# Kernel optimization log

Hardware: AMD Instinct MI355X
Metric: run time of the kernel (lower is better)

Reference implementation:

```python
import jax, jax.numpy as jnp
import numpy as np

B, S, D = 2, 1024, 4096          # batch, prefill seqlen, model dim
H, KVH, HD = 32, 8, 128          # q heads, kv heads, head dim
MAX = 2048                       # kv-cache capacity
THETA = 1000000.0
REP = H // KVH


def _rope_tables(pos):
    # pos: [S] int -> cos/sin [S, HD]
    inv_freq = 1.0 / (THETA ** (jnp.arange(0, HD, 2, dtype=jnp.float32) / HD))
    freqs = pos[:, None].astype(jnp.float32) * inv_freq[None, :]
    emb = jnp.concatenate([freqs, freqs], axis=-1)
    return jnp.cos(emb), jnp.sin(emb)


def _rotate_half(t):
    t1, t2 = jnp.split(t, 2, axis=-1)
    return jnp.concatenate([-t2, t1], axis=-1)


def setup_inputs() -> dict:
    key = jax.random.key(0)
    k = jax.random.split(key, 8)
    sc = 1.0 / np.sqrt(D)
    x = jax.random.normal(k[0], (B, S, D), jnp.float32)
    storage_idx = jnp.arange(S, dtype=jnp.int32)
    cache = jnp.zeros((2, 1, B, KVH, MAX, HD), jnp.float32)
    causal = jnp.tril(jnp.ones((MAX, MAX), bool))
    mask = jnp.where(causal, 0.0, -1e9).astype(jnp.float32)
    Wq = jax.random.normal(k[1], (D, H * HD), jnp.float32) * sc
    bq = jax.random.normal(k[2], (H * HD,), jnp.float32) * 0.01
    Wk = jax.random.normal(k[3], (D, KVH * HD), jnp.float32) * sc
    bk = jax.random.normal(k[4], (KVH * HD,), jnp.float32) * 0.01
    Wv = jax.random.normal(k[5], (D, KVH * HD), jnp.float32) * sc
    bv = jax.random.normal(k[6], (KVH * HD,), jnp.float32) * 0.01
    Wo = jax.random.normal(k[7], (H * HD, D), jnp.float32) * sc
    return {"x": x, "storage_idx": storage_idx, "cache": cache, "mask": mask,
            "Wq": Wq, "bq": bq, "Wk": Wk, "bk": bk, "Wv": Wv, "bv": bv, "Wo": Wo}


def reference(x, storage_idx, cache, mask, Wq, bq, Wk, bk, Wv, bv, Wo):
    bsz, seqlen, _ = x.shape
    # QKV projections -> [b, heads, s, hd]
    xq = (x @ Wq + bq).reshape(bsz, seqlen, H, HD).transpose(0, 2, 1, 3)
    xk = (x @ Wk + bk).reshape(bsz, seqlen, KVH, HD).transpose(0, 2, 1, 3)
    xv = (x @ Wv + bv).reshape(bsz, seqlen, KVH, HD).transpose(0, 2, 1, 3)
    # inline RoPE at positions storage_idx
    cos, sin = _rope_tables(storage_idx)       # [s, hd]
    cos = cos[None, None]                      # [1,1,s,hd]
    sin = sin[None, None]
    xq = xq * cos + _rotate_half(xq) * sin
    xk = xk * cos + _rotate_half(xk) * sin
    # KV-cache scatter (index_copy_ on dim -2 at storage_idx)
    keys = cache[0, 0].at[:, :, storage_idx, :].set(xk)    # [b, kvh, MAX, hd]
    values = cache[1, 0].at[:, :, storage_idx, :].set(xv)
    # GQA: repeat kv heads
    keys = jnp.repeat(keys, REP, axis=1)       # [b, H, MAX, hd]
    values = jnp.repeat(values, REP, axis=1)
    # attention with additive mask rows gathered at storage_idx
    scores = jnp.einsum('bhqd,bhkd->bhqk', xq, keys) / np.sqrt(HD)
    scores = scores + mask[storage_idx][None, None]        # [b, H, s, MAX]
    attn = jax.nn.softmax(scores, axis=-1)
    out = jnp.einsum('bhqk,bhkd->bhqd', attn, values)
    out = out.transpose(0, 2, 1, 3).reshape(bsz, seqlen, H * HD)
    return out @ Wo
```

## Files before the change

kernel.cpp:

```cpp
#include <hip/hip_runtime.h>
#include <hip/hip_bf16.h>

typedef unsigned short u16;
typedef unsigned int   u32;
using bf16x8 = __attribute__((ext_vector_type(8))) short;
using f32x4  = __attribute__((ext_vector_type(4))) float;
using f32x16 = __attribute__((ext_vector_type(16))) float;

#define AS1 __attribute__((address_space(1)))
#define AS3 __attribute__((address_space(3)))

static constexpr int S_   = 1024;
static constexpr int D_   = 4096;
static constexpr int H_   = 32;
static constexpr int KVH_ = 8;
static constexpr int HD_  = 128;
static constexpr int NQKV = H_*HD_ + 2*KVH_*HD_;

__device__ __forceinline__ u16 f2bf(float f) {
  union { float f; u32 u; } v; v.f = f;
  u32 r = v.u + 0x7FFFu + ((v.u >> 16) & 1u);
  return (u16)(r >> 16);
}

__global__ void k_convert(const float* __restrict__ src, u16* __restrict__ dst, int n4) {
  int i = blockIdx.x * blockDim.x + threadIdx.x;
  if (i >= n4) return;
  float4 v = ((const float4*)src)[i];
  ushort4 o;
  o.x = f2bf(v.x); o.y = f2bf(v.y); o.z = f2bf(v.z); o.w = f2bf(v.w);
  ((ushort4*)dst)[i] = o;
}

__global__ __launch_bounds__(256) void k_transpose_all(
    const float* __restrict__ Wq, const float* __restrict__ Wk,
    const float* __restrict__ Wv, const float* __restrict__ Wo,
    u16* __restrict__ WB, u16* __restrict__ WoT) {
  constexpr int K = 4096;
  __shared__ float t[64][65];
  int id = blockIdx.x;
  const float* src; u16* dst; int N, tx, ty, perm;
  if (id < 4096)      { src = Wq; dst = WB;                        N = 4096; tx = id & 63; ty = id >> 6; perm = 1; }
  else if (id < 5120) { id -= 4096; src = Wk; dst = WB + (size_t)4096*K; N = 1024; tx = id & 15; ty = id >> 4; perm = 1; }
  else if (id < 6144) { id -= 5120; src = Wv; dst = WB + (size_t)5120*K; N = 1024; tx = id & 15; ty = id >> 4; perm = 0; }
  else                { id -= 6144; src = Wo; dst = WoT;           N = 4096; tx = id & 63; ty = id >> 6; perm = 0; }
  int k0 = ty * 64, n0 = tx * 64;
  int tid = threadIdx.x;
  int srcb[4];
#pragma unroll
  for (int g = 0; g < 4; ++g) {
    int np = n0 + g*16;
    if (perm) {
      int f = (np >> 4) & 7, m = f >> 1;
      srcb[g] = (np & ~127) + ((f & 1) ? 64 + m*16 : m*16);
    } else srcb[g] = np;
  }
  int lr = tid >> 4;
  int lc = (tid & 15) * 4;
  int scol = srcb[lc >> 4] + (lc & 15);
#pragma unroll
  for (int i = 0; i < 4; ++i) {
    float4 v = *(const float4*)&src[(size_t)(k0 + lr + i*16) * N + scol];
    t[lc+0][lr + i*16] = v.x;
    t[lc+1][lr + i*16] = v.y;
    t[lc+2][lr + i*16] = v.z;
    t[lc+3][lr + i*16] = v.w;
  }
  __syncthreads();
  int wn = tid >> 3;
  int wk = (tid & 7) * 8;
#pragma unroll
  for (int i = 0; i < 2; ++i) {
    const float* row = &t[wn + i*32][wk];
    ushort4 a, b;
    a.x = f2bf(row[0]); a.y = f2bf(row[1]); a.z = f2bf(row[2]); a.w = f2bf(row[3]);
    b.x = f2bf(row[4]); b.y = f2bf(row[5]); b.z = f2bf(row[6]); b.w = f2bf(row[7]);
    u16* o = &dst[(size_t)(n0 + wn + i*32) * K + k0 + wk];
    *(ushort4*)o = a;
    *(ushort4*)(o + 4) = b;
  }
}

__global__ void k_transpose_v(const u16* __restrict__ src, u16* __restrict__ dst) {
  __shared__ u16 t[32][33];
  int bg = blockIdx.z;
  int s0 = blockIdx.x * 32, h0 = blockIdx.y * 32;
  src += (size_t)bg * S_ * HD_;
  dst += (size_t)bg * S_ * HD_;
  int tx = threadIdx.x, ty = threadIdx.y;
#pragma unroll
  for (int i = 0; i < 4; ++i)
    t[ty + i*8][tx] = src[(size_t)(s0 + ty + i*8) * HD_ + h0 + tx];
  __syncthreads();
#pragma unroll
  for (int i = 0; i < 4; ++i)
    dst[(size_t)(h0 + ty + i*8) * S_ + s0 + tx] = t[tx][ty + i*8];
}

__global__ void k_rope(const int* __restrict__ sidx, float* __restrict__ cosd,
                       float* __restrict__ sind) {
  int i = blockIdx.x * blockDim.x + threadIdx.x;
  int s = i >> 6, d = i & 63;
  float pos  = (float)sidx[s];
  float invf = expf(-0.21586735246819178f * (float)d);
  float ph   = pos * invf;
  cosd[i] = cosf(ph);
  sind[i] = sinf(ph);
}

#define BAR   __builtin_amdgcn_s_barrier()
#define SCHB  __builtin_amdgcn_sched_barrier(0)

__global__ __launch_bounds__(512, 2) void k_gemmq(
    const u16* __restrict__ A, const u16* __restrict__ Bt,
    const float* __restrict__ bq, const float* __restrict__ bk,
    const float* __restrict__ bv,
    const float* __restrict__ cosd, const float* __restrict__ sind,
    u16* __restrict__ qb, u16* __restrict__ kb, u16* __restrict__ vb)
{
  constexpr int K = 4096;
  constexpr int ABYT = 256*128, BBYT = 192*128, STEP = ABYT+BBYT;
  __shared__ __align__(16) char lds[2*STEP];

  const int cpx = (int)gridDim.x >> 3;
  const int wkid = ((int)blockIdx.x & 7)*cpx + ((int)blockIdx.x >> 3);
  const int NT = 32;
  const int m0 = (wkid / NT) * 256, n0 = (wkid % NT) * 192;
  const int tid = threadIdx.x, w = tid>>6, lane = tid&63;
  const int l15 = lane&15, l4 = lane>>4;
  const int wr = w>>1, wc = w&1;
  const int row0 = tid>>3;
  const int ss = (tid&7) ^ (row0&7);
  const int NK = K >> 6;

  f32x4 acc[4][6];
#pragma unroll
  for (int i = 0; i < 4; ++i)
#pragma unroll
    for (int j = 0; j < 6; ++j) acc[i][j] = (f32x4){0.f,0.f,0.f,0.f};

  bf16x8 af[2][2][2];
  bf16x8 bfr[2][3][2];

#define QCHUNK(kt_, part_, r0c_)                                              \
  __builtin_amdgcn_global_load_lds(                                           \
    (AS1 void*)(((part_) ? Bt + (size_t)(n0 + (r0c_) + row0)*K                \
                         : A  + (size_t)(m0 + (r0c_) + row0)*K)               \
                + (size_t)(kt_)*64 + ss*8),                                   \
    (AS3 void*)(lds + ((kt_)&1)*STEP + (part_)*ABYT + (r0c_)*128 + w*1024),   \
    16, 0, 0)

#define QSTAGE_A(kt_)  { QCHUNK(kt_,0,0); QCHUNK(kt_,0,64); QCHUNK(kt_,0,128); QCHUNK(kt_,0,192); }
#define QSTAGE_B(kt_)  { QCHUNK(kt_,1,0); QCHUNK(kt_,1,64); QCHUNK(kt_,1,128); }

#define QR_A(mh_, lA_)                                                        \
  _Pragma("unroll") for (int i2 = 0; i2 < 2; ++i2)                            \
  _Pragma("unroll") for (int kk = 0; kk < 2; ++kk) {                          \
    int row = wr*64 + ((mh_)*2 + i2)*16 + l15;                                \
    af[mh_][i2][kk] = *(const bf16x8*)((lA_) + row*128 + (((kk*4+l4) ^ (row&7)) << 4)); }

#define QR_B(nh_, lB_)                                                        \
  _Pragma("unroll") for (int jj = 0; jj < 3; ++jj)                            \
  _Pragma("unroll") for (int kk = 0; kk < 2; ++kk) {                          \
    int row = wc*96 + ((nh_)*3 + jj)*16 + l15;                                \
    bfr[nh_][jj][kk] = *(const bf16x8*)((lB_) + row*128 + (((kk*4+l4) ^ (row&7)) << 4)); }

#define QMFMA(mh_, nh_)                                                       \
  __builtin_amdgcn_s_setprio(1);                                              \
  _Pragma("unroll") for (int i2 = 0; i2 < 2; ++i2)                            \
  _Pragma("unroll") for (int jj = 0; jj < 3; ++jj)                            \
  _Pragma("unroll") for (int kk = 0; kk < 2; ++kk)                            \
    acc[(mh_)*2+i2][(nh_)*3+jj] = __builtin_amdgcn_mfma_f32_16x16x32_bf16(    \
        af[mh_][i2][kk], bfr[nh_][jj][kk], acc[(mh_)*2+i2][(nh_)*3+jj], 0, 0, 0); \
  __builtin_amdgcn_s_setprio(0);

  QSTAGE_A(0); QSTAGE_B(0);
  QSTAGE_A(1); QSTAGE_B(1);
  asm volatile("s_waitcnt vmcnt(7)" ::: "memory");
  BAR; SCHB;
  {
    const char* lA0 = lds;
    const char* lB0 = lds + ABYT;
    QR_A(0, lA0); QR_B(0, lB0);
  }

  for (int kt = 0; kt < NK; ++kt) {
    const char* lA = lds + (kt&1)*STEP;
    const char* lB = lA + ABYT;
    QR_B(1, lB);
    asm volatile("s_waitcnt lgkmcnt(6)" ::: "memory");
    SCHB;
    QMFMA(0,0);
    QR_A(1, lA);
    asm volatile("s_waitcnt lgkmcnt(4)" ::: "memory");
    BAR; SCHB;
    if (kt+2 < NK) QSTAGE_B(kt+2);
    QMFMA(0,1);
    asm volatile("s_waitcnt lgkmcnt(0)" ::: "memory");
    BAR; SCHB;
    if (kt+2 < NK) QSTAGE_A(kt+2);
    QMFMA(1,0);
    if (kt+1 < NK) {
      if (kt+2 < NK) asm volatile("s_waitcnt vmcnt(7)" ::: "memory");
      else           asm volatile("s_waitcnt vmcnt(0)" ::: "memory");
      BAR; SCHB;
      const char* lAn = lds + ((kt+1)&1)*STEP;
      const char* lBn = lAn + ABYT;
      QR_A(0, lAn); QR_B(0, lBn);
      SCHB;
    }
    QMFMA(1,1);
  }
#undef QCHUNK
#undef QSTAGE_A
#undef QSTAGE_B
#undef QR_A
#undef QR_B
#undef QMFMA

  const int cb16 = (n0 + wc*96) >> 4;
#pragma unroll
  for (int p = 0; p < 3; ++p) {
    int g0 = cb16 + 2*p;
    if (g0 < 320) {
      bool isQ = (g0 < 256);
      int gs = isQ ? g0 : g0 - 256;
      int h = gs >> 3, m = (gs & 7) >> 1;
      int dlo = m*16 + l15;
      const float* bias = isQ ? bq : bk;
      u16* dst = isQ ? qb : kb;
      int nheads = isQ ? H_ : KVH_;
      float scale = isQ ? 0.08838834764831845f : 1.0f;
      float b_lo = bias[h*128 + dlo];
      float b_hi = bias[h*128 + 64 + dlo];
#pragma unroll
      for (int i = 0; i < 4; ++i)
#pragma unroll
        for (int r = 0; r < 4; ++r) {
          int sr = m0 + wr*64 + i*16 + l4*4 + r;
          int b_ = sr >> 10, s_ = sr & 1023;
          float cs = cosd[s_*64 + dlo], sn = sind[s_*64 + dlo];
          float lo = acc[i][2*p][r]   + b_lo;
          float hi = acc[i][2*p+1][r] + b_hi;
          size_t obase = (((size_t)b_*nheads + h)*S_ + s_)*(size_t)HD_;
          dst[obase + dlo]      = f2bf((lo*cs - hi*sn) * scale);
          dst[obase + 64 + dlo] = f2bf((hi*cs + lo*sn) * scale);
        }
    } else {
#pragma unroll
      for (int q = 0; q < 2; ++q) {
        int gv = g0 + q - 320;
        int h = gv >> 3, d = (gv & 7)*16 + l15;
        float bbv = bv[h*128 + d];
#pragma unroll
        for (int i = 0; i < 4; ++i)
#pragma unroll
          for (int r = 0; r < 4; ++r) {
            int sr = m0 + wr*64 + i*16 + l4*4 + r;
            int b_ = sr >> 10, s_ = sr & 1023;
            size_t obase = (((size_t)b_*KVH_ + h)*S_ + s_)*(size_t)HD_;
            vb[obase + d] = f2bf(acc[i][2*p+q][r] + bbv);
          }
      }
    }
  }
}

__global__ __launch_bounds__(512, 2) void k_gemmo(
    const u16* __restrict__ A, const u16* __restrict__ Bt,
    float* __restrict__ C, int N, int K)
{
  constexpr int ABYT = 128*128, BBYT = 256*128, STEP = ABYT+BBYT;
  __shared__ __align__(16) char lds[2*STEP];

  const int cpx = (int)gridDim.x >> 3;
  const int wkid = ((int)blockIdx.x & 7)*cpx + ((int)blockIdx.x >> 3);
  const int NT = N / 256;
  const int m0 = (wkid / NT) * 128, n0 = (wkid % NT) * 256;
  const int tid = threadIdx.x, w = tid>>6, lane = tid&63;
  const int l31 = lane & 31, lh = lane >> 5;
  const int wr = w>>2, wc = w&3;
  const int row0 = tid>>3;
  const int ss = (tid&7) ^ (row0&7);
  const int NK = K >> 6;

  f32x16 acc00 = {}, acc01 = {}, acc10 = {}, acc11 = {};

  bf16x8 af[2][4];
  bf16x8 bfr[2][4];

#define OCHUNK(kt_, part_, r0c_)                                              \
  __builtin_amdgcn_global_load_lds(                                           \
    (AS1 void*)(((part_) ? Bt + (size_t)(n0 + (r0c_) + row0)*K                \
                         : A  + (size_t)(m0 + (r0c_) + row0)*K)               \
                + (size_t)(kt_)*64 + ss*8),                                   \
    (AS3 void*)(lds + ((kt_)&1)*STEP + (part_)*ABYT + (r0c_)*128 + w*1024),   \
    16, 0, 0)

#define OR_A(mh_, lA_)                                                        \
  _Pragma("unroll") for (int st = 0; st < 4; ++st) {                          \
    int row = wr*64 + (mh_)*32 + l31;                                         \
    af[mh_][st] = *(const bf16x8*)((lA_) + row*128 + ((((st*2)+lh) ^ (row&7)) << 4)); }

#define OR_B(nh_, lB_)                                                        \
  _Pragma("unroll") for (int st = 0; st < 4; ++st) {                          \
    int row = wc*64 + (nh_)*32 + l31;                                         \
    bfr[nh_][st] = *(const bf16x8*)((lB_) + row*128 + ((((st*2)+lh) ^ (row&7)) << 4)); }

#define OMFMA(mh_, nh_, accv_)                                                \
  __builtin_amdgcn_s_setprio(1);                                              \
  _Pragma("unroll") for (int st = 0; st < 4; ++st)                            \
    accv_ = __builtin_amdgcn_mfma_f32_32x32x16_bf16(af[mh_][st], bfr[nh_][st], accv_, 0, 0, 0); \
  __builtin_amdgcn_s_setprio(0);

  OCHUNK(0,0,0); OCHUNK(0,0,64);
  OCHUNK(0,1,0); OCHUNK(0,1,64); OCHUNK(0,1,128); OCHUNK(0,1,192);
  OCHUNK(1,0,0); OCHUNK(1,0,64);
  OCHUNK(1,1,0); OCHUNK(1,1,64); OCHUNK(1,1,128); OCHUNK(1,1,192);
  asm volatile("s_waitcnt vmcnt(6)" ::: "memory");
  BAR; SCHB;
  {
    const char* lA0 = lds;
    const char* lB0 = lds + ABYT;
    OR_A(0, lA0); OR_B(0, lB0);
  }

  for (int kt = 0; kt < NK; ++kt) {
    const char* lA = lds + (kt&1)*STEP;
    const char* lB = lA + ABYT;
    OR_B(1, lB);
    asm volatile("s_waitcnt lgkmcnt(4)" ::: "memory");
    SCHB;
    OMFMA(0,0, acc00);
    OR_A(1, lA);
    asm volatile("s_waitcnt lgkmcnt(4)" ::: "memory");
    BAR; SCHB;
    if (kt+2 < NK) { OCHUNK(kt+2,1,0); OCHUNK(kt+2,1,64); OCHUNK(kt+2,1,128); OCHUNK(kt+2,1,192); }
    OMFMA(0,1, acc01);
    asm volatile("s_waitcnt lgkmcnt(0)" ::: "memory");
    BAR; SCHB;
    if (kt+2 < NK) { OCHUNK(kt+2,0,0); OCHUNK(kt+2,0,64); }
    OMFMA(1,0, acc10);
    if (kt+1 < NK) {
      if (kt+2 < NK) asm volatile("s_waitcnt vmcnt(6)" ::: "memory");
      else           asm volatile("s_waitcnt vmcnt(0)" ::: "memory");
      BAR; SCHB;
      const char* lAn = lds + ((kt+1)&1)*STEP;
      const char* lBn = lAn + ABYT;
      OR_A(0, lAn); OR_B(0, lBn);
      SCHB;
    }
    OMFMA(1,1, acc11);
  }
#undef OCHUNK
#undef OR_A
#undef OR_B
#undef OMFMA

#define OWRITE(mh_, nh_, accv_)                                               \
  _Pragma("unroll") for (int r = 0; r < 16; ++r) {                            \
    int row = m0 + wr*64 + (mh_)*32 + (r & 3) + 8*(r >> 2) + 4*lh;            \
    int col = n0 + wc*64 + (nh_)*32 + l31;                                    \
    C[(size_t)row * N + col] = accv_[r]; }
  OWRITE(0,0, acc00); OWRITE(0,1, acc01); OWRITE(1,0, acc10); OWRITE(1,1, acc11);
#undef OWRITE
}

__global__ __launch_bounds__(256, 4) void k_attn(
    const u16* __restrict__ Q, const u16* __restrict__ Kc,
    const u16* __restrict__ Vt, u16* __restrict__ AO)
{
  __shared__ __align__(16) char Kls[2][16384];
  __shared__ __align__(16) char Vls[2][16384];
  __shared__ u16 Pl[4][1024];

  int id = blockIdx.x;
  int slot = id >> 3;
  int bg   = (id & 7)*2 + (slot & 1);
  int rem  = slot >> 1;
  int h_in = rem & 3, bx = rem >> 2;
  int b = bg >> 3, g = bg & 7, h = g*4 + h_in;
  int tA = bx, tB = 15 - bx;

  int tid = threadIdx.x, w = tid >> 6, lane = tid & 63;
  int l15 = lane & 15, l4 = lane >> 4;
  const u16* Qh = Q  + ((size_t)b*H_   + h) * S_ * HD_;
  const u16* Kp = Kc + ((size_t)b*KVH_ + g) * S_ * HD_;
  const u16* Vp = Vt + ((size_t)b*KVH_ + g) * (size_t)HD_ * S_;
  u16* AOh = AO + ((size_t)b*S_) * (H_*HD_) + h*HD_;
  char* Pw = (char*)&Pl[w][0];

  int kOff[4], vOff[4];
#pragma unroll
  for (int c = 0; c < 4; ++c) {
    int ci = c*256 + tid;
    int krow = ci >> 4, ks = ci & 15;
    kOff[c] = krow * HD_ + ((ks & 8) | ((ks & 7) ^ (krow & 7))) * 8;
    int vrow = ci >> 3, vs = ci & 7;
    vOff[c] = vrow * S_ + (vs ^ (vrow & 7)) * 8;
  }

#define ASTAGE(kv_, bb_) {                                                    \
    const u16* ks_ = Kp + (size_t)(kv_) * 64 * HD_;                           \
    const u16* vs_ = Vp + (size_t)(kv_) * 64;                                 \
    _Pragma("unroll") for (int c = 0; c < 4; ++c) {                           \
      __builtin_amdgcn_global_load_lds((AS1 void*)(ks_ + kOff[c]),            \
          (AS3 void*)(&Kls[bb_][0] + c*4096 + w*1024), 16, 0, 0);             \
      __builtin_amdgcn_global_load_lds((AS1 void*)(vs_ + vOff[c]),            \
          (AS3 void*)(&Vls[bb_][0] + c*4096 + w*1024), 16, 0, 0); } }

  bf16x8 qf[4];
#pragma unroll
  for (int kc = 0; kc < 4; ++kc)
    qf[kc] = *(const bf16x8*)(Qh + (size_t)(tA*64 + w*16 + l15)*HD_ + kc*32 + l4*8);

  f32x4 o[8];
#pragma unroll
  for (int n = 0; n < 8; ++n) o[n] = (f32x4){0.f,0.f,0.f,0.f};
  float mrow[4] = {-3e38f,-3e38f,-3e38f,-3e38f};
  float lrow[4] = {0.f,0.f,0.f,0.f};

  ASTAGE(0, 0);
  asm volatile("s_waitcnt vmcnt(0)" ::: "memory");
  __builtin_amdgcn_s_barrier();

  const int NIT = tA + tB + 2;
  int buf = 0;
  for (int it = 0; it < NIT; ++it) {
    bool phA = (it <= tA);
    int kv = phA ? it : it - tA - 1;
    int qt = phA ? tA : tB;
    if (it + 1 < NIT) {
      int kvn = (it + 1 <= tA) ? it + 1 : it - tA;
      ASTAGE(kvn, buf ^ 1);
    }
    const char* Ksb = &Kls[buf][0];
    const char* Vsb = &Vls[buf][0];

    f32x4 sc[4];
    __builtin_amdgcn_s_setprio(1);
#pragma unroll
    for (int ct = 0; ct < 4; ++ct) {
      f32x4 s4 = (f32x4){0.f,0.f,0.f,0.f};
#pragma unroll
      for (int kc = 0; kc < 4; ++kc) {
        int row = ct*16 + l15, s = kc*4 + l4;
        bf16x8 kf = *(const bf16x8*)(Ksb + row*256 + ((((s & 7) ^ (row & 7)) | (s & 8)) << 4));
        s4 = __builtin_amdgcn_mfma_f32_16x16x32_bf16(qf[kc], kf, s4, 0, 0, 0);
      }
      sc[ct] = s4;
    }
    __builtin_amdgcn_s_setprio(0);

    if (kv == qt) {
      int qrow0 = qt*64 + w*16;
#pragma unroll
      for (int ct = 0; ct < 4; ++ct)
#pragma unroll
        for (int r = 0; r < 4; ++r) {
          int col = kv*64 + ct*16 + l15;
          if (col > qrow0 + l4*4 + r) sc[ct][r] = -1e9f;
        }
    }

    float f[4];
#pragma unroll
    for (int r = 0; r < 4; ++r) {
      float mx = fmaxf(fmaxf(sc[0][r], sc[1][r]), fmaxf(sc[2][r], sc[3][r]));
      mx = fmaxf(mx, __shfl_xor(mx, 1));
      mx = fmaxf(mx, __shfl_xor(mx, 2));
      mx = fmaxf(mx, __shfl_xor(mx, 4));
      mx = fmaxf(mx, __shfl_xor(mx, 8));
      float nm = fmaxf(mrow[r], mx);
      f[r] = __expf(mrow[r] - nm);
      mrow[r] = nm;
    }
    float rs[4] = {0.f,0.f,0.f,0.f};
#pragma unroll
    for (int ct = 0; ct < 4; ++ct)
#pragma unroll
      for (int r = 0; r < 4; ++r) {
        float p = __expf(sc[ct][r] - mrow[r]);
        rs[r] += p;
        int row = l4*4 + r, col = ct*16 + l15;
        int byte = row*128 + (((col >> 3) ^ (row & 7)) << 4) + (col & 7)*2;
        *(u16*)(Pw + byte) = f2bf(p);
      }
#pragma unroll
    for (int r = 0; r < 4; ++r) {
      float sum = rs[r];
      sum += __shfl_xor(sum, 1);
      sum += __shfl_xor(sum, 2);
      sum += __shfl_xor(sum, 4);
      sum += __shfl_xor(sum, 8);
      lrow[r] = lrow[r]*f[r] + sum;
    }
#pragma unroll
    for (int n = 0; n < 8; ++n)
#pragma unroll
      for (int r = 0; r < 4; ++r) o[n][r] *= f[r];

    __builtin_amdgcn_s_setprio(1);
#pragma unroll
    for (int kk = 0; kk < 2; ++kk) {
      int pbyte = l15*128 + (((kk*4 + l4) ^ (l15 & 7)) << 4);
      bf16x8 pf = *(const bf16x8*)(Pw + pbyte);
#pragma unroll
      for (int n = 0; n < 8; ++n) {
        int vrow = n*16 + l15, s = kk*4 + l4;
        bf16x8 vf = *(const bf16x8*)(Vsb + vrow*128 + ((s ^ (vrow & 7)) << 4));
        o[n] = __builtin_amdgcn_mfma_f32_16x16x32_bf16(pf, vf, o[n], 0, 0, 0);
      }
    }
    __builtin_amdgcn_s_setprio(0);

    if (it == tA) {
#pragma unroll
      for (int n = 0; n < 8; ++n)
#pragma unroll
        for (int r = 0; r < 4; ++r) {
          int srow = tA*64 + w*16 + l4*4 + r;
          AOh[(size_t)srow * (H_*HD_) + n*16 + l15] = f2bf(o[n][r] / lrow[r]);
        }
#pragma unroll
      for (int n = 0; n < 8; ++n) o[n] = (f32x4){0.f,0.f,0.f,0.f};
#pragma unroll
      for (int r = 0; r < 4; ++r) { mrow[r] = -3e38f; lrow[r] = 0.f; }
#pragma unroll
      for (int kc = 0; kc < 4; ++kc)
        qf[kc] = *(const bf16x8*)(Qh + (size_t)(tB*64 + w*16 + l15)*HD_ + kc*32 + l4*8);
    }

    asm volatile("s_waitcnt vmcnt(0)" ::: "memory");
    __builtin_amdgcn_s_barrier();
    buf ^= 1;
  }
#undef ASTAGE

#pragma unroll
  for (int n = 0; n < 8; ++n)
#pragma unroll
    for (int r = 0; r < 4; ++r) {
      int srow = tB*64 + w*16 + l4*4 + r;
      AOh[(size_t)srow * (H_*HD_) + n*16 + l15] = f2bf(o[n][r] / lrow[r]);
    }
}

extern "C" void kernel_launch(void* const* d_in, const int* in_sizes, int n_in,
                              void* d_out, int out_size, void* d_ws, size_t ws_size,
                              hipStream_t stream) {
  (void)in_sizes; (void)n_in; (void)out_size; (void)ws_size;
  const float* x   = (const float*)d_in[0];
  const int*   sid = (const int*)  d_in[1];
  const float* Wq  = (const float*)d_in[4];
  const float* bq  = (const float*)d_in[5];
  const float* Wk  = (const float*)d_in[6];
  const float* bk  = (const float*)d_in[7];
  const float* Wv  = (const float*)d_in[8];
  const float* bv  = (const float*)d_in[9];
  const float* Wo  = (const float*)d_in[10];
  float* out = (float*)d_out;

  char* ws = (char*)d_ws;
  u16*   xb   = (u16*)  (ws);
  u16*   WB   = (u16*)  (ws + 16777216);
  u16*   WoT  = (u16*)  (ws + 67108864);
  u16*   qb   = (u16*)  (ws + 150994944);
  u16*   kb   = (u16*)  (ws + 167772160);
  u16*   vb   = (u16*)  (ws + 171966464);
  u16*   VT   = (u16*)  (ws + 176160768);
  float* cosd = (float*)(ws + 180355072);
  float* sind = (float*)(ws + 180617216);
  u16*   AO   = xb;

  dim3 tb(32, 8);
  k_convert<<<8192, 256, 0, stream>>>(x, xb, (2048*4096)/4);
  k_transpose_all<<<10240, 256, 0, stream>>>(Wq, Wk, Wv, Wo, WB, WoT);
  k_rope<<<256, 256, 0, stream>>>(sid, cosd, sind);
  k_gemmq<<<256, 512, 0, stream>>>(xb, WB, bq, bk, bv, cosd, sind, qb, kb, vb);
  k_transpose_v<<<dim3(32,4,16), tb, 0, stream>>>(vb, VT);
  k_attn<<<512, 256, 0, stream>>>(qb, kb, VT, AO);
  k_gemmo<<<256, 512, 0, stream>>>(AO, WoT, out, 4096, 4096);
}
```

Measured before the change: 282.3 us.

## Fuse prep kernels into one launch and reshape output GEMM tile to 256x128

Merges the x-to-bf16 conversion, the weight transposes and the RoPE table generation into a single k_prep kernel that dispatches on block index, removing two kernel launches and their gaps. Separately, the output projection GEMM tile changes from 128x256 to 256x128 (M by N), with the wave grid becoming 4x2 and the A/B staging counts swapped to match. The tile reshape changes how much of each operand is reused per block and the L2 access pattern, at the risk of a different balance between LDS traffic and MFMA work.

```diff
diff --git a/kernel.cpp b/kernel.cpp
--- a/kernel.cpp
+++ b/kernel.cpp
@@ -23,29 +23,40 @@
   return (u16)(r >> 16);
 }
 
-__global__ void k_convert(const float* __restrict__ src, u16* __restrict__ dst, int n4) {
-  int i = blockIdx.x * blockDim.x + threadIdx.x;
-  if (i >= n4) return;
-  float4 v = ((const float4*)src)[i];
-  ushort4 o;
-  o.x = f2bf(v.x); o.y = f2bf(v.y); o.z = f2bf(v.z); o.w = f2bf(v.w);
-  ((ushort4*)dst)[i] = o;
-}
-
-__global__ __launch_bounds__(256) void k_transpose_all(
+__global__ __launch_bounds__(256) void k_prep(
+    const float* __restrict__ x, u16* __restrict__ xb,
     const float* __restrict__ Wq, const float* __restrict__ Wk,
     const float* __restrict__ Wv, const float* __restrict__ Wo,
-    u16* __restrict__ WB, u16* __restrict__ WoT) {
+    u16* __restrict__ WB, u16* __restrict__ WoT,
+    const int* __restrict__ sidx, float* __restrict__ cosd, float* __restrict__ sind) {
   constexpr int K = 4096;
   __shared__ float t[64][65];
-  int id = blockIdx.x;
+  int bid = blockIdx.x, tid = threadIdx.x;
+  if (bid < 8192) {
+    int i = bid * 256 + tid;
+    float4 v = ((const float4*)x)[i];
+    ushort4 o;
+    o.x = f2bf(v.x); o.y = f2bf(v.y); o.z = f2bf(v.z); o.w = f2bf(v.w);
+    ((ushort4*)xb)[i] = o;
+    return;
+  }
+  if (bid >= 18432) {
+    int i = (bid - 18432) * 256 + tid;
+    int s = i >> 6, d = i & 63;
+    float pos  = (float)sidx[s];
+    float invf = expf(-0.21586735246819178f * (float)d);
+    float ph   = pos * invf;
+    cosd[i] = cosf(ph);
+    sind[i] = sinf(ph);
+    return;
+  }
+  int id = bid - 8192;
   const float* src; u16* dst; int N, tx, ty, perm;
   if (id < 4096)      { src = Wq; dst = WB;                        N = 4096; tx = id & 63; ty = id >> 6; perm = 1; }
   else if (id < 5120) { id -= 4096; src = Wk; dst = WB + (size_t)4096*K; N = 1024; tx = id & 15; ty = id >> 4; perm = 1; }
   else if (id < 6144) { id -= 5120; src = Wv; dst = WB + (size_t)5120*K; N = 1024; tx = id & 15; ty = id >> 4; perm = 0; }
   else                { id -= 6144; src = Wo; dst = WoT;           N = 4096; tx = id & 63; ty = id >> 6; perm = 0; }
   int k0 = ty * 64, n0 = tx * 64;
-  int tid = threadIdx.x;
   int srcb[4];
 #pragma unroll
   for (int g = 0; g < 4; ++g) {
@@ -95,17 +106,6 @@
 #pragma unroll
   for (int i = 0; i < 4; ++i)
     dst[(size_t)(h0 + ty + i*8) * S_ + s0 + tx] = t[tx][ty + i*8];
-}
-
-__global__ void k_rope(const int* __restrict__ sidx, float* __restrict__ cosd,
-                       float* __restrict__ sind) {
-  int i = blockIdx.x * blockDim.x + threadIdx.x;
-  int s = i >> 6, d = i & 63;
-  float pos  = (float)sidx[s];
-  float invf = expf(-0.21586735246819178f * (float)d);
-  float ph   = pos * invf;
-  cosd[i] = cosf(ph);
-  sind[i] = sinf(ph);
 }
 
 #define BAR   __builtin_amdgcn_s_barrier()
@@ -270,16 +270,16 @@
     const u16* __restrict__ A, const u16* __restrict__ Bt,
     float* __restrict__ C, int N, int K)
 {
-  constexpr int ABYT = 128*128, BBYT = 256*128, STEP = ABYT+BBYT;
+  constexpr int ABYT = 256*128, BBYT = 128*128, STEP = ABYT+BBYT;
   __shared__ __align__(16) char lds[2*STEP];
 
   const int cpx = (int)gridDim.x >> 3;
   const int wkid = ((int)blockIdx.x & 7)*cpx + ((int)blockIdx.x >> 3);
-  const int NT = N / 256;
-  const int m0 = (wkid / NT) * 128, n0 = (wkid % NT) * 256;
+  const int NT = N / 128;
+  const int m0 = (wkid / NT) * 256, n0 = (wkid % NT) * 128;
   const int tid = threadIdx.x, w = tid>>6, lane = tid&63;
   const int l31 = lane & 31, lh = lane >> 5;
-  const int wr = w>>2, wc = w&3;
+  const int wr = w>>1, wc = w&1;
   const int row0 = tid>>3;
   const int ss = (tid&7) ^ (row0&7);
   const int NK = K >> 6;
@@ -297,6 +297,9 @@
     (AS3 void*)(lds + ((kt_)&1)*STEP + (part_)*ABYT + (r0c_)*128 + w*1024),   \
     16, 0, 0)
 
+#define OSTAGE_A(kt_)  { OCHUNK(kt_,0,0); OCHUNK(kt_,0,64); OCHUNK(kt_,0,128); OCHUNK(kt_,0,192); }
+#define OSTAGE_B(kt_)  { OCHUNK(kt_,1,0); OCHUNK(kt_,1,64); }
+
 #define OR_A(mh_, lA_)                                                        \
   _Pragma("unroll") for (int st = 0; st < 4; ++st) {                          \
     int row = wr*64 + (mh_)*32 + l31;                                         \
@@ -313,10 +316,8 @@
     accv_ = __builtin_amdgcn_mfma_f32_32x32x16_bf16(af[mh_][st], bfr[nh_][st], accv_, 0, 0, 0); \
   __builtin_amdgcn_s_setprio(0);
 
-  OCHUNK(0,0,0); OCHUNK(0,0,64);
-  OCHUNK(0,1,0); OCHUNK(0,1,64); OCHUNK(0,1,128); OCHUNK(0,1,192);
-  OCHUNK(1,0,0); OCHUNK(1,0,64);
-  OCHUNK(1,1,0); OCHUNK(1,1,64); OCHUNK(1,1,128); OCHUNK(1,1,192);
+  OSTAGE_A(0); OSTAGE_B(0);
+  OSTAGE_A(1); OSTAGE_B(1);
   asm volatile("s_waitcnt vmcnt(6)" ::: "memory");
   BAR; SCHB;
   {
@@ -335,11 +336,11 @@
     OR_A(1, lA);
     asm volatile("s_waitcnt lgkmcnt(4)" ::: "memory");
     BAR; SCHB;
-    if (kt+2 < NK) { OCHUNK(kt+2,1,0); OCHUNK(kt+2,1,64); OCHUNK(kt+2,1,128); OCHUNK(kt+2,1,192); }
+    if (kt+2 < NK) OSTAGE_B(kt+2);
     OMFMA(0,1, acc01);
     asm volatile("s_waitcnt lgkmcnt(0)" ::: "memory");
     BAR; SCHB;
-    if (kt+2 < NK) { OCHUNK(kt+2,0,0); OCHUNK(kt+2,0,64); }
+    if (kt+2 < NK) OSTAGE_A(kt+2);
     OMFMA(1,0, acc10);
     if (kt+1 < NK) {
       if (kt+2 < NK) asm volatile("s_waitcnt vmcnt(6)" ::: "memory");
@@ -353,6 +354,8 @@
     OMFMA(1,1, acc11);
   }
 #undef OCHUNK
+#undef OSTAGE_A
+#undef OSTAGE_B
 #undef OR_A
 #undef OR_B
 #undef OMFMA
@@ -574,9 +577,7 @@
   u16*   AO   = xb;
 
   dim3 tb(32, 8);
-  k_convert<<<8192, 256, 0, stream>>>(x, xb, (2048*4096)/4);
-  k_transpose_all<<<10240, 256, 0, stream>>>(Wq, Wk, Wv, Wo, WB, WoT);
-  k_rope<<<256, 256, 0, stream>>>(sid, cosd, sind);
+  k_prep<<<18688, 256, 0, stream>>>(x, xb, Wq, Wk, Wv, Wo, WB, WoT, sid, cosd, sind);
   k_gemmq<<<256, 512, 0, stream>>>(xb, WB, bq, bk, bv, cosd, sind, qb, kb, vb);
   k_transpose_v<<<dim3(32,4,16), tb, 0, stream>>>(vb, VT);
   k_attn<<<512, 256, 0, stream>>>(qb, kb, VT, AO);
```

New measurement: 279.5 us. Within noise of the previous version (-1.0%).
